# Performance work log

Hardware: AMD Instinct MI355X
Metric: run time of the kernel (lower is better)

## Reference

```python
import jax, jax.numpy as jnp
import numpy as np

N_NODES = 50000


def gcn_conv(x, W, b, row, col, n):
    """PyG GCNConv with default add_self_loops=True, normalize=True.
    out[i] = sum_{e: col[e]=i} d^-1/2[row[e]] d^-1/2[i] * (x@W)[row[e]]
             + d^-1[i]*(x@W)[i] + b,  where d = in-degree + 1 (self-loop).
    """
    x_lin = x @ W                                   # [n, out_ch]
    ones = jnp.ones(row.shape[0], dtype=x.dtype)
    deg = jax.ops.segment_sum(ones, col, num_segments=n) + 1.0  # self-loop
    dinv = jax.lax.rsqrt(deg)                       # deg >= 1, safe
    norm = dinv[row] * dinv[col]                    # [E]
    msg = norm[:, None] * x_lin[row]                # [E, out_ch]
    agg = jax.ops.segment_sum(msg, col, num_segments=n)
    self_term = (dinv * dinv)[:, None] * x_lin      # self-loop contribution
    return agg + self_term + b


def setup_inputs() -> dict:
    key = jax.random.key(0)
    ks = jax.random.split(key, 10)
    in_ch, hid, out_ch = 128, 256, 64
    E = 800000
    x = jax.random.normal(ks[0], (N_NODES, in_ch), dtype=jnp.float32)
    edge_attr = jax.random.normal(ks[1], (E, 8), dtype=jnp.float32)  # unused by forward
    edge_index = jax.random.randint(ks[2], (2, E), 0, N_NODES, dtype=jnp.int64)
    def glorot(k, fan_in, fan_out):
        s = float(np.sqrt(6.0 / (fan_in + fan_out)))
        return jax.random.uniform(k, (fan_in, fan_out), jnp.float32, -s, s)
    return {
        "x": x,
        "edge_attr": edge_attr,
        "edge_index": edge_index,
        "W1": glorot(ks[3], in_ch, hid), "b1": jnp.zeros((hid,), jnp.float32),
        "W2": glorot(ks[4], hid, hid),  "b2": jnp.zeros((hid,), jnp.float32),
        "W3": glorot(ks[5], hid, out_ch), "b3": jnp.zeros((out_ch,), jnp.float32),
    }


def reference(x, edge_attr, edge_index, W1, b1, W2, b2, W3, b3):
    n = x.shape[0]
    row, col = edge_index[0], edge_index[1]
    h = jax.nn.sigmoid(gcn_conv(x, W1, b1, row, col, n))
    h = jax.nn.sigmoid(gcn_conv(h, W2, b2, row, col, n))
    # dropout(p=0.1) in eval mode is identity
    return gcn_conv(h, W3, b3, row, col, n)
```

## Files before the change

kernel.cpp:

```cpp
#include <hip/hip_runtime.h>
#include <hip/hip_bf16.h>

typedef __bf16 bf16x8_t __attribute__((ext_vector_type(8)));
typedef float f32x4_t __attribute__((ext_vector_type(4)));
typedef float f32x2_t __attribute__((ext_vector_type(2)));

__device__ __forceinline__ float bits2f(unsigned int u) {
    union { unsigned int u; float f; } c; c.u = u; return c.f;
}
__device__ __forceinline__ unsigned short f2bf_bits(float f) {
    __hip_bfloat16 h = __float2bfloat16(f);
    return __builtin_bit_cast(unsigned short, h);
}
__device__ __forceinline__ f32x2_t unpack_bf2(unsigned int u) {
    return (f32x2_t){bits2f(u << 16), bits2f(u & 0xffff0000u)};
}

__global__ void sentinel_fill(float* __restrict__ out, int n) {
    int i = blockIdx.x * blockDim.x + threadIdx.x;
    if (i < n) out[i] = 100.0f;
}

__global__ void detect_ei(const unsigned int* __restrict__ ei, int* __restrict__ flags) {
    int lane = threadIdx.x;
    int cz = 0;
    #pragma unroll
    for (int j = 0; j < 4; ++j) {
        int idx = lane * 4 + j;
        cz += (ei[2 * idx + 1] == 0u);
    }
    #pragma unroll
    for (int off = 32; off; off >>= 1) cz += __shfl_down(cz, off);
    if (lane == 0) flags[0] = (cz > 200);
}


__global__ void count_rank_dual(const int* __restrict__ ei, int* __restrict__ cnt,
                                int* __restrict__ rank, int E, int M,
                                const int* __restrict__ flags) {
    int e = blockIdx.x * blockDim.x + threadIdx.x;
    if (e < E) {
        int c = flags[0] ? ei[2 * E + 2 * e] : ei[E + e];
        int rk = 0;
        if ((unsigned)c < (unsigned)M) rk = atomicAdd(&cnt[c], 1);
        rank[e] = rk;
    }
}

__global__ void scan_blocks(const int* __restrict__ cnt, int* __restrict__ excl,
                            int* __restrict__ bsum, int n) {
    int tid = threadIdx.x;
    int i = blockIdx.x * 256 + tid;
    int lane = tid & 63, wv = tid >> 6;
    __shared__ int ws[4];
    int v = (i < n) ? cnt[i] : 0;
    int s = v;
    #pragma unroll
    for (int off = 1; off < 64; off <<= 1) {
        int t = __shfl_up(s, off);
        if (lane >= off) s += t;
    }
    if (lane == 63) ws[wv] = s;
    __syncthreads();
    if (tid == 0) { int a = 0; for (int q = 0; q < 4; ++q) { int t = ws[q]; ws[q] = a; a += t; } }
    __syncthreads();
    int ex = s - v + ws[wv];
    if (i < n) excl[i] = ex;
    if (tid == 255) bsum[blockIdx.x] = ex + v;
}

__global__ void scan_bsums(const int* __restrict__ bsum, int* __restrict__ boff,
                           int nb, int* __restrict__ colptr, int n) {
    int tid = threadIdx.x, lane = tid & 63, wv = tid >> 6;
    __shared__ int ws[4];
    __shared__ int carry;
    if (tid == 0) carry = 0;
    __syncthreads();
    for (int base = 0; base < nb; base += 256) {
        int i = base + tid;
        int v = (i < nb) ? bsum[i] : 0;
        int s = v;
        #pragma unroll
        for (int off = 1; off < 64; off <<= 1) {
            int t = __shfl_up(s, off);
            if (lane >= off) s += t;
        }
        if (lane == 63) ws[wv] = s;
        __syncthreads();
        if (tid == 0) { int a = carry; for (int q = 0; q < 4; ++q) { int t = ws[q]; ws[q] = a; a += t; } carry = a; }
        __syncthreads();
        int ex = s - v + ws[wv];
        if (i < nb) boff[i] = ex;
        __syncthreads();
    }
    if (tid == 0) colptr[n] = carry;
}

__global__ void scan_add_dinv(const int* __restrict__ excl, const int* __restrict__ boff,
                              const int* __restrict__ cnt, int* __restrict__ colptr,
                              float* __restrict__ dinv, int n) {
    int i = blockIdx.x * 256 + threadIdx.x;
    if (i < n) {
        colptr[i] = excl[i] + boff[blockIdx.x];
        dinv[i] = rsqrtf((float)cnt[i] + 1.0f);
    }
}

__global__ void fill_csr_part(const int* __restrict__ ei, const int* __restrict__ colptr,
                              const int* __restrict__ rank, int* __restrict__ esrc,
                              int E, int M, int psz, const int* __restrict__ flags) {
    int part = blockIdx.x & 7;
    int e = (blockIdx.x >> 3) * 256 + threadIdx.x;
    int lo = part * psz;
    int hi = lo + psz; if (hi > M) hi = M;
    if (e < E) {
        int r, c;
        if (flags[0]) { r = ei[2 * e]; c = ei[2 * E + 2 * e]; }
        else          { r = ei[e];     c = ei[E + e]; }
        if (c >= lo && c < hi && (unsigned)r < (unsigned)M) {
            int p = colptr[c] + rank[e];
            if ((unsigned)p < (unsigned)E) esrc[p] = r;
        }
    }
}

__global__ void transpose_all(const float* __restrict__ W1, const float* __restrict__ W2,
                              const float* __restrict__ W3,
                              unsigned short* __restrict__ Wt1, unsigned short* __restrict__ Wt2,
                              unsigned short* __restrict__ Wt3) {
    int i = blockIdx.x * 256 + threadIdx.x;
    if (i < 32768) {
        int k = i >> 8, n = i & 255;
        Wt1[n * 128 + k] = f2bf_bits(W1[i]);
    } else if (i < 32768 + 65536) {
        int j = i - 32768;
        int k = j >> 8, n = j & 255;
        Wt2[n * 256 + k] = f2bf_bits(W2[j]);
    } else if (i < 114688) {
        int j = i - 98304;
        int k = j >> 6, n = j & 63;
        Wt3[n * 256 + k] = f2bf_bits(W3[j]);
    }
}

__global__ void prescale_x(const float* __restrict__ x, const float* __restrict__ dinv,
                           unsigned short* __restrict__ xs, int total) {
    int i = blockIdx.x * 256 + threadIdx.x;
    if (i < total) {
        int row = i >> 7;
        xs[i] = f2bf_bits(x[i] * dinv[row]);
    }
}

template<int K, int BN, int NTOT, int EPI>
__global__ __launch_bounds__(256) void gemm_tile(
    const __bf16* __restrict__ A,
    const unsigned short* __restrict__ Bt,
    const float* __restrict__ dinv,
    const float* __restrict__ bias,
    void* __restrict__ Y,
    int M)
{
    constexpr int KS = (K > 128) ? 128 : K;
    constexpr int KP = KS + 8;
    constexpr int NT = BN / 2 / 16;
    __shared__ unsigned short Bs[BN * KP];

    const int tid  = threadIdx.x;
    const int lane = tid & 63;
    const int wave = tid >> 6;
    const int wm   = wave >> 1;
    const int wn   = wave & 1;
    const int quad = lane >> 4;
    const int l16  = lane & 15;
    const int n0   = blockIdx.y * BN;

    int mrow[4];
#pragma unroll
    for (int mt = 0; mt < 4; ++mt) {
        int r = blockIdx.x * 128 + wm * 64 + mt * 16 + l16;
        mrow[mt] = (r < M) ? r : (M - 1);
    }

    f32x4_t acc[4][NT];
#pragma unroll
    for (int mt = 0; mt < 4; ++mt)
#pragma unroll
        for (int t = 0; t < NT; ++t) acc[mt][t] = (f32x4_t){0.f, 0.f, 0.f, 0.f};

    const unsigned short* BsW = &Bs[(wn * (BN / 2)) * KP];

    for (int kh = 0; kh < K; kh += KS) {
        constexpr int CH = BN * KS / 8;
        for (int idx = tid; idx < CH; idx += 256) {
            int n  = idx / (KS / 8);
            int k8 = idx - n * (KS / 8);
            uint4 v = *(const uint4*)(Bt + (size_t)(n0 + n) * K + kh + k8 * 8);
            *(uint4*)&Bs[n * KP + k8 * 8] = v;
        }
        __syncthreads();

#pragma unroll
        for (int kc = 0; kc < KS; kc += 32) {
            bf16x8_t a[4], b[NT];
#pragma unroll
            for (int mt = 0; mt < 4; ++mt)
                a[mt] = *(const bf16x8_t*)(A + (size_t)mrow[mt] * K + kh + kc + quad * 8);
#pragma unroll
            for (int t = 0; t < NT; ++t)
                b[t] = *(const bf16x8_t*)&BsW[(t * 16 + l16) * KP + kc + quad * 8];
#pragma unroll
            for (int mt = 0; mt < 4; ++mt)
#pragma unroll
                for (int t = 0; t < NT; ++t)
                    acc[mt][t] = __builtin_amdgcn_mfma_f32_16x16x32_bf16(a[mt], b[t], acc[mt][t], 0, 0, 0);
        }
        if (kh + KS < K) __syncthreads();
    }

    float bv[NT];
    if constexpr (EPI == 1) {
#pragma unroll
        for (int t = 0; t < NT; ++t)
            bv[t] = bias[n0 + wn * (BN / 2) + t * 16 + l16];
    }

#pragma unroll
    for (int mt = 0; mt < 4; ++mt) {
        int rowbase = blockIdx.x * 128 + wm * 64 + mt * 16 + quad * 4;
#pragma unroll
        for (int r = 0; r < 4; ++r) {
            int rrow = rowbase + r;
            if (rrow < M) {
                if constexpr (EPI == 0) {
                    float dv = dinv[rrow];
#pragma unroll
                    for (int t = 0; t < NT; ++t) {
                        int ccol = n0 + wn * (BN / 2) + t * 16 + l16;
                        ((__hip_bfloat16*)Y)[(size_t)rrow * NTOT + ccol] =
                            __float2bfloat16(acc[mt][t][r] * dv);
                    }
                } else if constexpr (EPI == 1) {
#pragma unroll
                    for (int t = 0; t < NT; ++t) {
                        int ccol = n0 + wn * (BN / 2) + t * 16 + l16;
                        float o = acc[mt][t][r] + bv[t];
                        o = 1.f / (1.f + __expf(-o));
                        ((__hip_bfloat16*)Y)[(size_t)rrow * NTOT + ccol] = __float2bfloat16(o);
                    }
                } else {
                    float dv = dinv[rrow];
#pragma unroll
                    for (int t = 0; t < NT; ++t) {
                        int ccol = n0 + wn * (BN / 2) + t * 16 + l16;
                        float o = acc[mt][t][r] * dv;
                        int pk = __builtin_amdgcn_cvt_pk_fp8_f32(o, o, 0, false);
                        ((unsigned char*)Y)[(size_t)rrow * NTOT + ccol] = (unsigned char)(pk & 0xff);
                    }
                }
            }
        }
    }
}

__global__ __launch_bounds__(256) void aggregate_fp8_v2(
    const unsigned char* __restrict__ Y8,
    const int* __restrict__ colptr,
    const int* __restrict__ esrc,
    const float* __restrict__ dinv,
    const float* __restrict__ bias,
    unsigned short* __restrict__ H,
    int M, int Etot)
{
    const int lane = threadIdx.x & 63;
    const int wave = threadIdx.x >> 6;
    int node = blockIdx.x * 4 + wave;
    if (node >= M) return;

    int s = colptr[node];
    int e = colptr[node + 1];
    if (s < 0) s = 0;
    if (e > Etot) e = Etot;
    if (e < s) e = s;

    const char* Yb = (const char*)Y8;
    const unsigned lb = (unsigned)(lane * 4);

    f32x2_t a0 = {0.f, 0.f}, a1 = {0.f, 0.f};

    {
        unsigned u = *(const unsigned*)(Yb + (((unsigned)node) << 8) + lb);
        a0 += __builtin_amdgcn_cvt_pk_f32_fp8(u, false);
        a1 += __builtin_amdgcn_cvt_pk_f32_fp8(u, true);
    }
#pragma unroll 4
    for (int t = s; t < e; ++t) {
        unsigned off = (((unsigned)esrc[t]) << 8) + lb;
        unsigned u = *(const unsigned*)(Yb + off);
        a0 += __builtin_amdgcn_cvt_pk_f32_fp8(u, false);
        a1 += __builtin_amdgcn_cvt_pk_f32_fp8(u, true);
    }

    float dv = dinv[node];
    float4 bv = *(const float4*)(bias + lane * 4);
    float o0 = a0[0] * dv + bv.x;
    float o1 = a0[1] * dv + bv.y;
    float o2 = a1[0] * dv + bv.z;
    float o3 = a1[1] * dv + bv.w;
    o0 = 1.f / (1.f + __expf(-o0));
    o1 = 1.f / (1.f + __expf(-o1));
    o2 = 1.f / (1.f + __expf(-o2));
    o3 = 1.f / (1.f + __expf(-o3));
    uint2 st;
    st.x = (unsigned)f2bf_bits(o0) | ((unsigned)f2bf_bits(o1) << 16);
    st.y = (unsigned)f2bf_bits(o2) | ((unsigned)f2bf_bits(o3) << 16);
    *(uint2*)(H + (size_t)node * 256 + lane * 4) = st;
}

__global__ __launch_bounds__(256) void aggregate_bf16_128_v2(
    const unsigned short* __restrict__ Yin,
    const int* __restrict__ colptr,
    const int* __restrict__ esrc,
    const float* __restrict__ dinv,
    unsigned short* __restrict__ Hout,
    int M, int Etot)
{
    const int lane = threadIdx.x & 63;
    const int wave = threadIdx.x >> 6;
    int node = blockIdx.x * 4 + wave;
    if (node >= M) return;

    int s = colptr[node];
    int e = colptr[node + 1];
    if (s < 0) s = 0;
    if (e > Etot) e = Etot;
    if (e < s) e = s;

    const char* Yb = (const char*)Yin;
    const unsigned lb = (unsigned)(lane * 4);

    f32x2_t a = {0.f, 0.f};
    {
        unsigned u = *(const unsigned*)(Yb + (((unsigned)node) << 8) + lb);
        a += unpack_bf2(u);
    }
#pragma unroll 4
    for (int t = s; t < e; ++t) {
        unsigned off = (((unsigned)esrc[t]) << 8) + lb;
        unsigned u = *(const unsigned*)(Yb + off);
        a += unpack_bf2(u);
    }

    float dv = dinv[node];
    unsigned st = (unsigned)f2bf_bits(a[0] * dv) | ((unsigned)f2bf_bits(a[1] * dv) << 16);
    *(unsigned*)((char*)Hout + (size_t)node * 256 + lane * 4) = st;
}

__global__ __launch_bounds__(256) void aggregate_bf16_64_f32(
    const unsigned short* __restrict__ Yin,
    const int* __restrict__ colptr,
    const int* __restrict__ esrc,
    const float* __restrict__ dinv,
    const float* __restrict__ bias,
    float* __restrict__ out,
    int M, int Etot)
{
    const int lane = threadIdx.x & 63;
    const int wave = threadIdx.x >> 6;
    const int l5 = lane & 31;
    const int g  = lane >> 5;
    int node = blockIdx.x * 4 + wave;
    if (node >= M) return;

    int s = colptr[node];
    int e = colptr[node + 1];
    if (s < 0) s = 0;
    if (e > Etot) e = Etot;
    if (e < s) e = s;

    const char* Yb = (const char*)Yin;
    const unsigned lb = (unsigned)(l5 * 4);

    f32x2_t a = {0.f, 0.f};
    if (g == 0) {
        unsigned u = *(const unsigned*)(Yb + (((unsigned)node) << 7) + lb);
        a += unpack_bf2(u);
    }
#pragma unroll 4
    for (int t = s + g; t < e; t += 2) {
        unsigned off = (((unsigned)esrc[t]) << 7) + lb;
        unsigned u = *(const unsigned*)(Yb + off);
        a += unpack_bf2(u);
    }

    a[0] += __shfl_xor(a[0], 32);
    a[1] += __shfl_xor(a[1], 32);

    if (g == 0) {
        float dv = dinv[node];
        float2 bv = *(const float2*)(bias + l5 * 2);
        float2 st;
        st.x = a[0] * dv + bv.x;
        st.y = a[1] * dv + bv.y;
        *(float2*)(out + (size_t)node * 64 + l5 * 2) = st;
    }
}


extern "C" void kernel_launch(void* const* d_in, const int* in_sizes, int n_in,
                              void* d_out, int out_size, void* d_ws, size_t ws_size,
                              hipStream_t stream)
{
    int iEI = 2, iW1 = 3, iB1 = 4, iW2 = 5, iB2 = 6, iW3 = 7, iB3 = 8;
    if (n_in == 8) { iEI = 1; iW1 = 2; iB1 = 3; iW2 = 4; iB2 = 5; iW3 = 6; iB3 = 7; }

    const float* x  = (const float*)d_in[0];
    const int* ei   = (const int*)d_in[iEI];
    const float* W1 = (const float*)d_in[iW1];
    const float* b1 = (const float*)d_in[iB1];
    const float* W2 = (const float*)d_in[iW2];
    const float* b2 = (const float*)d_in[iB2];
    const float* W3 = (const float*)d_in[iW3];
    const float* b3 = (const float*)d_in[iB3];

    const int M = in_sizes[0] / 128;
    const int E = in_sizes[iEI] / 2;
    const int NB = (M + 255) / 256;
    const int PSZ = (M + 7) / 8;

    auto rnd = [](size_t b) { return (b + 255) & ~(size_t)255; };
    size_t needed = rnd(64 * 4)
                  + rnd((size_t)M * 4) * 2
                  + rnd((size_t)(M + 1) * 4)
                  + rnd((size_t)M * 4)
                  + rnd((size_t)(NB + 1) * 4) * 2
                  + rnd((size_t)E * 4) * 2
                  + rnd((size_t)256 * 128 * 2)
                  + rnd((size_t)256 * 256 * 2)
                  + rnd((size_t)64 * 256 * 2)
                  + rnd((size_t)M * 256 * 2) * 2;
    if (ws_size < needed) {
        sentinel_fill<<<(out_size + 255) / 256, 256, 0, stream>>>((float*)d_out, out_size);
        return;
    }

    char* p = (char*)d_ws;
    auto alloc = [&](size_t bytes) {
        char* r = p;
        p += (bytes + 255) & ~(size_t)255;
        return r;
    };
    int* flags  = (int*)alloc(64 * 4);
    float* dinv = (float*)alloc((size_t)M * 4);
    int* cnt    = (int*)alloc((size_t)M * 4);
    int* colptr = (int*)alloc((size_t)(M + 1) * 4);
    int* excl   = (int*)alloc((size_t)M * 4);
    int* bsum   = (int*)alloc((size_t)(NB + 1) * 4);
    int* boff   = (int*)alloc((size_t)(NB + 1) * 4);
    int* esrc   = (int*)alloc((size_t)E * 4);
    int* rank   = (int*)alloc((size_t)E * 4);
    unsigned short* Wt1 = (unsigned short*)alloc((size_t)256 * 128 * 2);
    unsigned short* Wt2 = (unsigned short*)alloc((size_t)256 * 256 * 2);
    unsigned short* Wt3 = (unsigned short*)alloc((size_t)64 * 256 * 2);
    __hip_bfloat16* ybuf = (__hip_bfloat16*)alloc((size_t)M * 256 * 2);
    __hip_bfloat16* hbuf = (__hip_bfloat16*)alloc((size_t)M * 256 * 2);

    unsigned short* xs = (unsigned short*)ybuf;
    unsigned short* xa = (unsigned short*)ybuf + (size_t)M * 128;
    unsigned char*  y8 = (unsigned char*)ybuf;

    detect_ei<<<1, 64, 0, stream>>>((const unsigned int*)ei, flags);

    hipMemsetAsync(cnt, 0, (size_t)M * 4, stream);
    count_rank_dual<<<(E + 255) / 256, 256, 0, stream>>>(ei, cnt, rank, E, M, flags);
    scan_blocks<<<NB, 256, 0, stream>>>(cnt, excl, bsum, M);
    scan_bsums<<<1, 256, 0, stream>>>(bsum, boff, NB, colptr, M);
    scan_add_dinv<<<NB, 256, 0, stream>>>(excl, boff, cnt, colptr, dinv, M);
    fill_csr_part<<<((E + 255) / 256) * 8, 256, 0, stream>>>(
        ei, colptr, rank, esrc, E, M, PSZ, flags);
    transpose_all<<<(114688 + 255) / 256, 256, 0, stream>>>(W1, W2, W3, Wt1, Wt2, Wt3);

    int gmb = (M + 127) / 128;
    int ga  = (M + 3) / 4;

    prescale_x<<<((M * 128) + 255) / 256, 256, 0, stream>>>(x, dinv, xs, M * 128);
    aggregate_bf16_128_v2<<<ga, 256, 0, stream>>>(
        xs, colptr, esrc, dinv, xa, M, E);
    gemm_tile<128, 128, 256, 1><<<dim3(gmb, 2), 256, 0, stream>>>(
        (const __bf16*)xa, Wt1, dinv, b1, hbuf, M);
    gemm_tile<256, 128, 256, 2><<<dim3(gmb, 2), 256, 0, stream>>>(
        (const __bf16*)hbuf, Wt2, dinv, b2, y8, M);
    aggregate_fp8_v2<<<ga, 256, 0, stream>>>(
        y8, colptr, esrc, dinv, b2, (unsigned short*)hbuf, M, E);
    gemm_tile<256, 64, 64, 0><<<dim3(gmb, 1), 256, 0, stream>>>(
        (const __bf16*)hbuf, Wt3, dinv, b3, ybuf, M);
    aggregate_bf16_64_f32<<<ga, 256, 0, stream>>>(
        (const unsigned short*)ybuf, colptr, esrc, dinv, b3, (float*)d_out, M, E);
}
```

Before: 343.9 us.

## Split gather features into 128-byte column chunks and parallelize edges within waves

```diff
diff --git a/kernel.cpp b/kernel.cpp
--- a/kernel.cpp
+++ b/kernel.cpp
@@ -14,6 +14,12 @@
 }
 __device__ __forceinline__ f32x2_t unpack_bf2(unsigned int u) {
     return (f32x2_t){bits2f(u << 16), bits2f(u & 0xffff0000u)};
+}
+__device__ __forceinline__ f32x2_t xsw(f32x2_t v, int off) {
+    f32x2_t r;
+    r[0] = __shfl_xor(v[0], off);
+    r[1] = __shfl_xor(v[1], off);
+    return r;
 }
 
 __global__ void sentinel_fill(float* __restrict__ out, int n) {
@@ -35,12 +41,17 @@
 }
 
 
-__global__ void count_rank_dual(const int* __restrict__ ei, int* __restrict__ cnt,
-                                int* __restrict__ rank, int E, int M,
-                                const int* __restrict__ flags) {
+__global__ void count_rank_dual2(const int* __restrict__ ei, int* __restrict__ cnt,
+                                 int* __restrict__ rank, int* __restrict__ c32,
+                                 int* __restrict__ r32, int E, int M,
+                                 const int* __restrict__ flags) {
     int e = blockIdx.x * blockDim.x + threadIdx.x;
     if (e < E) {
-        int c = flags[0] ? ei[2 * E + 2 * e] : ei[E + e];
+        int r, c;
+        if (flags[0]) { r = ei[2 * e]; c = ei[2 * E + 2 * e]; }
+        else          { r = ei[e];     c = ei[E + e]; }
+        c32[e] = c;
+        r32[e] = r;
         int rk = 0;
         if ((unsigned)c < (unsigned)M) rk = atomicAdd(&cnt[c], 1);
         rank[e] = rk;
@@ -106,20 +117,21 @@
     }
 }
 
-__global__ void fill_csr_part(const int* __restrict__ ei, const int* __restrict__ colptr,
-                              const int* __restrict__ rank, int* __restrict__ esrc,
-                              int E, int M, int psz, const int* __restrict__ flags) {
+__global__ void fill_csr_part2(const int* __restrict__ c32, const int* __restrict__ r32,
+                               const int* __restrict__ colptr, const int* __restrict__ rank,
+                               int* __restrict__ esrc, int E, int M, int psz) {
     int part = blockIdx.x & 7;
     int e = (blockIdx.x >> 3) * 256 + threadIdx.x;
     int lo = part * psz;
     int hi = lo + psz; if (hi > M) hi = M;
     if (e < E) {
-        int r, c;
-        if (flags[0]) { r = ei[2 * e]; c = ei[2 * E + 2 * e]; }
-        else          { r = ei[e];     c = ei[E + e]; }
-        if (c >= lo && c < hi && (unsigned)r < (unsigned)M) {
-            int p = colptr[c] + rank[e];
-            if ((unsigned)p < (unsigned)E) esrc[p] = r;
+        int c = c32[e];
+        if (c >= lo && c < hi) {
+            int r = r32[e];
+            if ((unsigned)r < (unsigned)M) {
+                int p = colptr[c] + rank[e];
+                if ((unsigned)p < (unsigned)E) esrc[p] = r;
+            }
         }
     }
 }
@@ -144,11 +156,13 @@
 }
 
 __global__ void prescale_x(const float* __restrict__ x, const float* __restrict__ dinv,
-                           unsigned short* __restrict__ xs, int total) {
+                           unsigned short* __restrict__ xs, int M, int total) {
     int i = blockIdx.x * 256 + threadIdx.x;
     if (i < total) {
         int row = i >> 7;
-        xs[i] = f2bf_bits(x[i] * dinv[row]);
+        int k = i & 127;
+        xs[(size_t)(k >> 6) * ((size_t)M * 64) + (size_t)row * 64 + (k & 63)] =
+            f2bf_bits(x[i] * dinv[row]);
     }
 }
 
@@ -255,7 +269,9 @@
                         int ccol = n0 + wn * (BN / 2) + t * 16 + l16;
                         float o = acc[mt][t][r] * dv;
                         int pk = __builtin_amdgcn_cvt_pk_fp8_f32(o, o, 0, false);
-                        ((unsigned char*)Y)[(size_t)rrow * NTOT + ccol] = (unsigned char)(pk & 0xff);
+                        size_t choff = (size_t)(ccol >> 7) * ((size_t)M * 128)
+                                     + (size_t)rrow * 128 + (ccol & 127);
+                        ((unsigned char*)Y)[choff] = (unsigned char)(pk & 0xff);
                     }
                 }
             }
@@ -263,18 +279,23 @@
     }
 }
 
-__global__ __launch_bounds__(256) void aggregate_fp8_v2(
-    const unsigned char* __restrict__ Y8,
+__global__ __launch_bounds__(256) void aggregate_fp8_c2(
+    const unsigned char* __restrict__ Y8c,
     const int* __restrict__ colptr,
     const int* __restrict__ esrc,
     const float* __restrict__ dinv,
     const float* __restrict__ bias,
     unsigned short* __restrict__ H,
-    int M, int Etot)
+    int M, int Etot, int nbx)
 {
     const int lane = threadIdx.x & 63;
     const int wave = threadIdx.x >> 6;
-    int node = blockIdx.x * 4 + wave;
+    const int sub = lane & 15;
+    const int grp = lane >> 4;
+    int bx = blockIdx.x;
+    int chunk = (bx >= nbx) ? 1 : 0;
+    if (chunk) bx -= nbx;
+    int node = bx * 4 + wave;
     if (node >= M) return;
 
     int s = colptr[node];
@@ -282,52 +303,70 @@
     if (s < 0) s = 0;
     if (e > Etot) e = Etot;
     if (e < s) e = s;
-
-    const char* Yb = (const char*)Y8;
-    const unsigned lb = (unsigned)(lane * 4);
-
-    f32x2_t a0 = {0.f, 0.f}, a1 = {0.f, 0.f};
-
-    {
-        unsigned u = *(const unsigned*)(Yb + (((unsigned)node) << 8) + lb);
-        a0 += __builtin_amdgcn_cvt_pk_f32_fp8(u, false);
-        a1 += __builtin_amdgcn_cvt_pk_f32_fp8(u, true);
-    }
-#pragma unroll 4
-    for (int t = s; t < e; ++t) {
-        unsigned off = (((unsigned)esrc[t]) << 8) + lb;
-        unsigned u = *(const unsigned*)(Yb + off);
-        a0 += __builtin_amdgcn_cvt_pk_f32_fp8(u, false);
-        a1 += __builtin_amdgcn_cvt_pk_f32_fp8(u, true);
-    }
-
-    float dv = dinv[node];
-    float4 bv = *(const float4*)(bias + lane * 4);
-    float o0 = a0[0] * dv + bv.x;
-    float o1 = a0[1] * dv + bv.y;
-    float o2 = a1[0] * dv + bv.z;
-    float o3 = a1[1] * dv + bv.w;
-    o0 = 1.f / (1.f + __expf(-o0));
-    o1 = 1.f / (1.f + __expf(-o1));
-    o2 = 1.f / (1.f + __expf(-o2));
-    o3 = 1.f / (1.f + __expf(-o3));
-    uint2 st;
-    st.x = (unsigned)f2bf_bits(o0) | ((unsigned)f2bf_bits(o1) << 16);
-    st.y = (unsigned)f2bf_bits(o2) | ((unsigned)f2bf_bits(o3) << 16);
-    *(uint2*)(H + (size_t)node * 256 + lane * 4) = st;
-}
-
-__global__ __launch_bounds__(256) void aggregate_bf16_128_v2(
-    const unsigned short* __restrict__ Yin,
+    int n = e - s;
+
+    const char* Yb = (const char*)(Y8c + (size_t)chunk * ((size_t)M * 128));
+    const unsigned lb = (unsigned)(sub * 8);
+
+    f32x2_t a0 = {0.f, 0.f}, a1 = {0.f, 0.f}, a2 = {0.f, 0.f}, a3 = {0.f, 0.f};
+
+    if (grp == 0) {
+        uint2 u = *(const uint2*)(Yb + ((unsigned)node) * 128u + lb);
+        a0 += __builtin_amdgcn_cvt_pk_f32_fp8(u.x, false);
+        a1 += __builtin_amdgcn_cvt_pk_f32_fp8(u.x, true);
+        a2 += __builtin_amdgcn_cvt_pk_f32_fp8(u.y, false);
+        a3 += __builtin_amdgcn_cvt_pk_f32_fp8(u.y, true);
+    }
+#pragma unroll 2
+    for (int t = grp; t < n; t += 4) {
+        unsigned off = ((unsigned)esrc[s + t]) * 128u + lb;
+        uint2 u = *(const uint2*)(Yb + off);
+        a0 += __builtin_amdgcn_cvt_pk_f32_fp8(u.x, false);
+        a1 += __builtin_amdgcn_cvt_pk_f32_fp8(u.x, true);
+        a2 += __builtin_amdgcn_cvt_pk_f32_fp8(u.y, false);
+        a3 += __builtin_amdgcn_cvt_pk_f32_fp8(u.y, true);
+    }
+
+    a0 += xsw(a0, 16); a1 += xsw(a1, 16); a2 += xsw(a2, 16); a3 += xsw(a3, 16);
+    a0 += xsw(a0, 32); a1 += xsw(a1, 32); a2 += xsw(a2, 32); a3 += xsw(a3, 32);
+
+    if (grp == 0) {
+        float dv = dinv[node];
+        int chb = chunk * 128 + sub * 8;
+        float4 b0 = *(const float4*)(bias + chb);
+        float4 b1 = *(const float4*)(bias + chb + 4);
+        float o[8];
+        o[0] = a0[0] * dv + b0.x; o[1] = a0[1] * dv + b0.y;
+        o[2] = a1[0] * dv + b0.z; o[3] = a1[1] * dv + b0.w;
+        o[4] = a2[0] * dv + b1.x; o[5] = a2[1] * dv + b1.y;
+        o[6] = a3[0] * dv + b1.z; o[7] = a3[1] * dv + b1.w;
+        #pragma unroll
+        for (int k = 0; k < 8; ++k) o[k] = 1.f / (1.f + __expf(-o[k]));
+        uint4 st;
+        st.x = (unsigned)f2bf_bits(o[0]) | ((unsigned)f2bf_bits(o[1]) << 16);
+        st.y = (unsigned)f2bf_bits(o[2]) | ((unsigned)f2bf_bits(o[3]) << 16);
+        st.z = (unsigned)f2bf_bits(o[4]) | ((unsigned)f2bf_bits(o[5]) << 16);
+        st.w = (unsigned)f2bf_bits(o[6]) | ((unsigned)f2bf_bits(o[7]) << 16);
+        *(uint4*)(H + (size_t)node * 256 + chb) = st;
+    }
+}
+
+__global__ __launch_bounds__(256) void aggregate_bf16_c2(
+    const unsigned short* __restrict__ Xc,
     const int* __restrict__ colptr,
     const int* __restrict__ esrc,
     const float* __restrict__ dinv,
     unsigned short* __restrict__ Hout,
-    int M, int Etot)
+    int M, int Etot, int nbx)
 {
     const int lane = threadIdx.x & 63;
     const int wave = threadIdx.x >> 6;
-    int node = blockIdx.x * 4 + wave;
+    const int sub = lane & 15;
+    const int grp = lane >> 4;
+    int bx = blockIdx.x;
+    int chunk = (bx >= nbx) ? 1 : 0;
+    if (chunk) bx -= nbx;
+    int node = bx * 4 + wave;
     if (node >= M) return;
 
     int s = colptr[node];
@@ -335,28 +374,39 @@
     if (s < 0) s = 0;
     if (e > Etot) e = Etot;
     if (e < s) e = s;
-
-    const char* Yb = (const char*)Yin;
-    const unsigned lb = (unsigned)(lane * 4);
-
-    f32x2_t a = {0.f, 0.f};
-    {
-        unsigned u = *(const unsigned*)(Yb + (((unsigned)node) << 8) + lb);
-        a += unpack_bf2(u);
-    }
-#pragma unroll 4
-    for (int t = s; t < e; ++t) {
-        unsigned off = (((unsigned)esrc[t]) << 8) + lb;
-        unsigned u = *(const unsigned*)(Yb + off);
-        a += unpack_bf2(u);
-    }
-
-    float dv = dinv[node];
-    unsigned st = (unsigned)f2bf_bits(a[0] * dv) | ((unsigned)f2bf_bits(a[1] * dv) << 16);
-    *(unsigned*)((char*)Hout + (size_t)node * 256 + lane * 4) = st;
-}
-
-__global__ __launch_bounds__(256) void aggregate_bf16_64_f32(
+    int n = e - s;
+
+    const char* Yb = (const char*)(Xc + (size_t)chunk * ((size_t)M * 64));
+    const unsigned lb = (unsigned)(sub * 8);
+
+    f32x2_t a0 = {0.f, 0.f}, a1 = {0.f, 0.f};
+
+    if (grp == 0) {
+        uint2 u = *(const uint2*)(Yb + ((unsigned)node) * 128u + lb);
+        a0 += unpack_bf2(u.x);
+        a1 += unpack_bf2(u.y);
+    }
+#pragma unroll 2
+    for (int t = grp; t < n; t += 4) {
+        unsigned off = ((unsigned)esrc[s + t]) * 128u + lb;
+        uint2 u = *(const uint2*)(Yb + off);
+        a0 += unpack_bf2(u.x);
+        a1 += unpack_bf2(u.y);
+    }
+
+    a0 += xsw(a0, 16); a1 += xsw(a1, 16);
+    a0 += xsw(a0, 32); a1 += xsw(a1, 32);
+
+    if (grp == 0) {
+        float dv = dinv[node];
+        uint2 st;
+        st.x = (unsigned)f2bf_bits(a0[0] * dv) | ((unsigned)f2bf_bits(a0[1] * dv) << 16);
+        st.y = (unsigned)f2bf_bits(a1[0] * dv) | ((unsigned)f2bf_bits(a1[1] * dv) << 16);
+        *(uint2*)(Hout + (size_t)node * 128 + chunk * 64 + sub * 4) = st;
+    }
+}
+
+__global__ __launch_bounds__(256) void aggregate_bf16_64_v3(
     const unsigned short* __restrict__ Yin,
     const int* __restrict__ colptr,
     const int* __restrict__ esrc,
@@ -367,8 +417,8 @@
 {
     const int lane = threadIdx.x & 63;
     const int wave = threadIdx.x >> 6;
-    const int l5 = lane & 31;
-    const int g  = lane >> 5;
+    const int sub = lane & 15;
+    const int grp = lane >> 4;
     int node = blockIdx.x * 4 + wave;
     if (node >= M) return;
 
@@ -377,32 +427,38 @@
     if (s < 0) s = 0;
     if (e > Etot) e = Etot;
     if (e < s) e = s;
+    int n = e - s;
 
     const char* Yb = (const char*)Yin;
-    const unsigned lb = (unsigned)(l5 * 4);
-
-    f32x2_t a = {0.f, 0.f};
-    if (g == 0) {
-        unsigned u = *(const unsigned*)(Yb + (((unsigned)node) << 7) + lb);
-        a += unpack_bf2(u);
-    }
-#pragma unroll 4
-    for (int t = s + g; t < e; t += 2) {
-        unsigned off = (((unsigned)esrc[t]) << 7) + lb;
-        unsigned u = *(const unsigned*)(Yb + off);
-        a += unpack_bf2(u);
-    }
-
-    a[0] += __shfl_xor(a[0], 32);
-    a[1] += __shfl_xor(a[1], 32);
-
-    if (g == 0) {
+    const unsigned lb = (unsigned)(sub * 8);
+
+    f32x2_t a0 = {0.f, 0.f}, a1 = {0.f, 0.f};
+
+    if (grp == 0) {
+        uint2 u = *(const uint2*)(Yb + ((unsigned)node) * 128u + lb);
+        a0 += unpack_bf2(u.x);
+        a1 += unpack_bf2(u.y);
+    }
+#pragma unroll 2
+    for (int t = grp; t < n; t += 4) {
+        unsigned off = ((unsigned)esrc[s + t]) * 128u + lb;
+        uint2 u = *(const uint2*)(Yb + off);
+        a0 += unpack_bf2(u.x);
+        a1 += unpack_bf2(u.y);
+    }
+
+    a0 += xsw(a0, 16); a1 += xsw(a1, 16);
+    a0 += xsw(a0, 32); a1 += xsw(a1, 32);
+
+    if (grp == 0) {
         float dv = dinv[node];
-        float2 bv = *(const float2*)(bias + l5 * 2);
-        float2 st;
-        st.x = a[0] * dv + bv.x;
-        st.y = a[1] * dv + bv.y;
-        *(float2*)(out + (size_t)node * 64 + l5 * 2) = st;
+        float4 bv = *(const float4*)(bias + sub * 4);
+        float4 st;
+        st.x = a0[0] * dv + bv.x;
+        st.y = a0[1] * dv + bv.y;
+        st.z = a1[0] * dv + bv.z;
+        st.w = a1[1] * dv + bv.w;
+        *(float4*)(out + (size_t)node * 64 + sub * 4) = st;
     }
 }
 
@@ -434,7 +490,7 @@
                   + rnd((size_t)(M + 1) * 4)
                   + rnd((size_t)M * 4)
                   + rnd((size_t)(NB + 1) * 4) * 2
-                  + rnd((size_t)E * 4) * 2
+                  + rnd((size_t)E * 4) * 4
                   + rnd((size_t)256 * 128 * 2)
                   + rnd((size_t)256 * 256 * 2)
                   + rnd((size_t)64 * 256 * 2)
@@ -459,6 +515,8 @@
     int* boff   = (int*)alloc((size_t)(NB + 1) * 4);
     int* esrc   = (int*)alloc((size_t)E * 4);
     int* rank   = (int*)alloc((size_t)E * 4);
+    int* c32    = (int*)alloc((size_t)E * 4);
+    int* r32    = (int*)alloc((size_t)E * 4);
     unsigned short* Wt1 = (unsigned short*)alloc((size_t)256 * 128 * 2);
     unsigned short* Wt2 = (unsigned short*)alloc((size_t)256 * 256 * 2);
     unsigned short* Wt3 = (unsigned short*)alloc((size_t)64 * 256 * 2);
@@ -472,28 +530,28 @@
     detect_ei<<<1, 64, 0, stream>>>((const unsigned int*)ei, flags);
 
     hipMemsetAsync(cnt, 0, (size_t)M * 4, stream);
-    count_rank_dual<<<(E + 255) / 256, 256, 0, stream>>>(ei, cnt, rank, E, M, flags);
+    count_rank_dual2<<<(E + 255) / 256, 256, 0, stream>>>(ei, cnt, rank, c32, r32, E, M, flags);
     scan_blocks<<<NB, 256, 0, stream>>>(cnt, excl, bsum, M);
     scan_bsums<<<1, 256, 0, stream>>>(bsum, boff, NB, colptr, M);
     scan_add_dinv<<<NB, 256, 0, stream>>>(excl, boff, cnt, colptr, dinv, M);
-    fill_csr_part<<<((E + 255) / 256) * 8, 256, 0, stream>>>(
-        ei, colptr, rank, esrc, E, M, PSZ, flags);
+    fill_csr_part2<<<((E + 255) / 256) * 8, 256, 0, stream>>>(
+        c32, r32, colptr, rank, esrc, E, M, PSZ);
     transpose_all<<<(114688 + 255) / 256, 256, 0, stream>>>(W1, W2, W3, Wt1, Wt2, Wt3);
 
     int gmb = (M + 127) / 128;
     int ga  = (M + 3) / 4;
 
-    prescale_x<<<((M * 128) + 255) / 256, 256, 0, stream>>>(x, dinv, xs, M * 128);
-    aggregate_bf16_128_v2<<<ga, 256, 0, stream>>>(
-        xs, colptr, esrc, dinv, xa, M, E);
+    prescale_x<<<((M * 128) + 255) / 256, 256, 0, stream>>>(x, dinv, xs, M, M * 128);
+    aggregate_bf16_c2<<<2 * ga, 256, 0, stream>>>(
+        xs, colptr, esrc, dinv, xa, M, E, ga);
     gemm_tile<128, 128, 256, 1><<<dim3(gmb, 2), 256, 0, stream>>>(
         (const __bf16*)xa, Wt1, dinv, b1, hbuf, M);
     gemm_tile<256, 128, 256, 2><<<dim3(gmb, 2), 256, 0, stream>>>(
         (const __bf16*)hbuf, Wt2, dinv, b2, y8, M);
-    aggregate_fp8_v2<<<ga, 256, 0, stream>>>(
-        y8, colptr, esrc, dinv, b2, (unsigned short*)hbuf, M, E);
+    aggregate_fp8_c2<<<2 * ga, 256, 0, stream>>>(
+        y8, colptr, esrc, dinv, b2, (unsigned short*)hbuf, M, E, ga);
     gemm_tile<256, 64, 64, 0><<<dim3(gmb, 1), 256, 0, stream>>>(
         (const __bf16*)hbuf, Wt3, dinv, b3, ybuf, M);
-    aggregate_bf16_64_f32<<<ga, 256, 0, stream>>>(
+    aggregate_bf16_64_v3<<<ga, 256, 0, stream>>>(
         (const unsigned short*)ybuf, colptr, esrc, dinv, b3, (float*)d_out, M, E);
 }
```

Result: slower. 369.8 us (+7.5%).

## Software-pipeline neighbor gathers in aggregation kernels and cache int32 edge indices

Applied to the files above, without the earlier changes.

```diff
diff --git a/kernel.cpp b/kernel.cpp
--- a/kernel.cpp
+++ b/kernel.cpp
@@ -35,12 +35,17 @@
 }
 
 
-__global__ void count_rank_dual(const int* __restrict__ ei, int* __restrict__ cnt,
-                                int* __restrict__ rank, int E, int M,
-                                const int* __restrict__ flags) {
+__global__ void count_rank_dual2(const int* __restrict__ ei, int* __restrict__ cnt,
+                                 int* __restrict__ rank, int* __restrict__ c32,
+                                 int* __restrict__ r32, int E, int M,
+                                 const int* __restrict__ flags) {
     int e = blockIdx.x * blockDim.x + threadIdx.x;
     if (e < E) {
-        int c = flags[0] ? ei[2 * E + 2 * e] : ei[E + e];
+        int r, c;
+        if (flags[0]) { r = ei[2 * e]; c = ei[2 * E + 2 * e]; }
+        else          { r = ei[e];     c = ei[E + e]; }
+        c32[e] = c;
+        r32[e] = r;
         int rk = 0;
         if ((unsigned)c < (unsigned)M) rk = atomicAdd(&cnt[c], 1);
         rank[e] = rk;
@@ -106,20 +111,21 @@
     }
 }
 
-__global__ void fill_csr_part(const int* __restrict__ ei, const int* __restrict__ colptr,
-                              const int* __restrict__ rank, int* __restrict__ esrc,
-                              int E, int M, int psz, const int* __restrict__ flags) {
+__global__ void fill_csr_part2(const int* __restrict__ c32, const int* __restrict__ r32,
+                               const int* __restrict__ colptr, const int* __restrict__ rank,
+                               int* __restrict__ esrc, int E, int M, int psz) {
     int part = blockIdx.x & 7;
     int e = (blockIdx.x >> 3) * 256 + threadIdx.x;
     int lo = part * psz;
     int hi = lo + psz; if (hi > M) hi = M;
     if (e < E) {
-        int r, c;
-        if (flags[0]) { r = ei[2 * e]; c = ei[2 * E + 2 * e]; }
-        else          { r = ei[e];     c = ei[E + e]; }
-        if (c >= lo && c < hi && (unsigned)r < (unsigned)M) {
-            int p = colptr[c] + rank[e];
-            if ((unsigned)p < (unsigned)E) esrc[p] = r;
+        int c = c32[e];
+        if (c >= lo && c < hi) {
+            int r = r32[e];
+            if ((unsigned)r < (unsigned)M) {
+                int p = colptr[c] + rank[e];
+                if ((unsigned)p < (unsigned)E) esrc[p] = r;
+            }
         }
     }
 }
@@ -263,7 +269,7 @@
     }
 }
 
-__global__ __launch_bounds__(256) void aggregate_fp8_v2(
+__global__ __launch_bounds__(256) void aggregate_fp8_v4(
     const unsigned char* __restrict__ Y8,
     const int* __restrict__ colptr,
     const int* __restrict__ esrc,
@@ -282,24 +288,58 @@
     if (s < 0) s = 0;
     if (e > Etot) e = Etot;
     if (e < s) e = s;
+    int n = e - s;
 
     const char* Yb = (const char*)Y8;
     const unsigned lb = (unsigned)(lane * 4);
 
+    unsigned su = *(const unsigned*)(Yb + (((unsigned)node) << 8) + lb);
+
     f32x2_t a0 = {0.f, 0.f}, a1 = {0.f, 0.f};
 
-    {
-        unsigned u = *(const unsigned*)(Yb + (((unsigned)node) << 8) + lb);
-        a0 += __builtin_amdgcn_cvt_pk_f32_fp8(u, false);
-        a1 += __builtin_amdgcn_cvt_pk_f32_fp8(u, true);
-    }
-#pragma unroll 4
-    for (int t = s; t < e; ++t) {
-        unsigned off = (((unsigned)esrc[t]) << 8) + lb;
+    auto gather8 = [&](unsigned* u, int base) {
+        #pragma unroll
+        for (int k = 0; k < 8; ++k) {
+            unsigned off = (((unsigned)esrc[s + base + k]) << 8) + lb;
+            u[k] = *(const unsigned*)(Yb + off);
+        }
+    };
+    auto acc8 = [&](const unsigned* u) {
+        #pragma unroll
+        for (int k = 0; k < 8; ++k) {
+            a0 += __builtin_amdgcn_cvt_pk_f32_fp8(u[k], false);
+            a1 += __builtin_amdgcn_cvt_pk_f32_fp8(u[k], true);
+        }
+    };
+
+    unsigned ua[8], ub[8];
+    int NB = n >> 3;
+    if (NB > 0) {
+        gather8(ua, 0);
+        int i = 1;
+        for (; i + 1 < NB; i += 2) {
+            gather8(ub, i << 3);
+            acc8(ua);
+            gather8(ua, (i + 1) << 3);
+            acc8(ub);
+        }
+        if (i < NB) {
+            gather8(ub, i << 3);
+            acc8(ua);
+            acc8(ub);
+        } else {
+            acc8(ua);
+        }
+    }
+    #pragma unroll 2
+    for (int t = NB << 3; t < n; ++t) {
+        unsigned off = (((unsigned)esrc[s + t]) << 8) + lb;
         unsigned u = *(const unsigned*)(Yb + off);
         a0 += __builtin_amdgcn_cvt_pk_f32_fp8(u, false);
         a1 += __builtin_amdgcn_cvt_pk_f32_fp8(u, true);
     }
+    a0 += __builtin_amdgcn_cvt_pk_f32_fp8(su, false);
+    a1 += __builtin_amdgcn_cvt_pk_f32_fp8(su, true);
 
     float dv = dinv[node];
     float4 bv = *(const float4*)(bias + lane * 4);
@@ -317,7 +357,7 @@
     *(uint2*)(H + (size_t)node * 256 + lane * 4) = st;
 }
 
-__global__ __launch_bounds__(256) void aggregate_bf16_128_v2(
+__global__ __launch_bounds__(256) void aggregate_bf16_128_v4(
     const unsigned short* __restrict__ Yin,
     const int* __restrict__ colptr,
     const int* __restrict__ esrc,
@@ -335,28 +375,60 @@
     if (s < 0) s = 0;
     if (e > Etot) e = Etot;
     if (e < s) e = s;
+    int n = e - s;
 
     const char* Yb = (const char*)Yin;
     const unsigned lb = (unsigned)(lane * 4);
 
+    unsigned su = *(const unsigned*)(Yb + (((unsigned)node) << 8) + lb);
+
     f32x2_t a = {0.f, 0.f};
-    {
-        unsigned u = *(const unsigned*)(Yb + (((unsigned)node) << 8) + lb);
-        a += unpack_bf2(u);
-    }
-#pragma unroll 4
-    for (int t = s; t < e; ++t) {
-        unsigned off = (((unsigned)esrc[t]) << 8) + lb;
+
+    auto gather8 = [&](unsigned* u, int base) {
+        #pragma unroll
+        for (int k = 0; k < 8; ++k) {
+            unsigned off = (((unsigned)esrc[s + base + k]) << 8) + lb;
+            u[k] = *(const unsigned*)(Yb + off);
+        }
+    };
+    auto acc8 = [&](const unsigned* u) {
+        #pragma unroll
+        for (int k = 0; k < 8; ++k) a += unpack_bf2(u[k]);
+    };
+
+    unsigned ua[8], ub[8];
+    int NB = n >> 3;
+    if (NB > 0) {
+        gather8(ua, 0);
+        int i = 1;
+        for (; i + 1 < NB; i += 2) {
+            gather8(ub, i << 3);
+            acc8(ua);
+            gather8(ua, (i + 1) << 3);
+            acc8(ub);
+        }
+        if (i < NB) {
+            gather8(ub, i << 3);
+            acc8(ua);
+            acc8(ub);
+        } else {
+            acc8(ua);
+        }
+    }
+    #pragma unroll 2
+    for (int t = NB << 3; t < n; ++t) {
+        unsigned off = (((unsigned)esrc[s + t]) << 8) + lb;
         unsigned u = *(const unsigned*)(Yb + off);
         a += unpack_bf2(u);
     }
+    a += unpack_bf2(su);
 
     float dv = dinv[node];
     unsigned st = (unsigned)f2bf_bits(a[0] * dv) | ((unsigned)f2bf_bits(a[1] * dv) << 16);
     *(unsigned*)((char*)Hout + (size_t)node * 256 + lane * 4) = st;
 }
 
-__global__ __launch_bounds__(256) void aggregate_bf16_64_f32(
+__global__ __launch_bounds__(256) void aggregate_bf16_64_v4(
     const unsigned short* __restrict__ Yin,
     const int* __restrict__ colptr,
     const int* __restrict__ esrc,
@@ -377,21 +449,53 @@
     if (s < 0) s = 0;
     if (e > Etot) e = Etot;
     if (e < s) e = s;
+    int n = e - s;
 
     const char* Yb = (const char*)Yin;
     const unsigned lb = (unsigned)(l5 * 4);
 
+    unsigned su = 0;
+    if (g == 0) su = *(const unsigned*)(Yb + (((unsigned)node) << 7) + lb);
+
     f32x2_t a = {0.f, 0.f};
-    if (g == 0) {
-        unsigned u = *(const unsigned*)(Yb + (((unsigned)node) << 7) + lb);
-        a += unpack_bf2(u);
-    }
-#pragma unroll 4
-    for (int t = s + g; t < e; t += 2) {
-        unsigned off = (((unsigned)esrc[t]) << 7) + lb;
+
+    auto gather4 = [&](unsigned* u, int base) {
+        #pragma unroll
+        for (int k = 0; k < 4; ++k) {
+            unsigned off = (((unsigned)esrc[s + base + 2 * k + g]) << 7) + lb;
+            u[k] = *(const unsigned*)(Yb + off);
+        }
+    };
+    auto acc4 = [&](const unsigned* u) {
+        #pragma unroll
+        for (int k = 0; k < 4; ++k) a += unpack_bf2(u[k]);
+    };
+
+    unsigned ua[4], ub[4];
+    int NB = n >> 3;
+    if (NB > 0) {
+        gather4(ua, 0);
+        int i = 1;
+        for (; i + 1 < NB; i += 2) {
+            gather4(ub, i << 3);
+            acc4(ua);
+            gather4(ua, (i + 1) << 3);
+            acc4(ub);
+        }
+        if (i < NB) {
+            gather4(ub, i << 3);
+            acc4(ua);
+            acc4(ub);
+        } else {
+            acc4(ua);
+        }
+    }
+    for (int t = NB << 3; t + g < n; t += 2) {
+        unsigned off = (((unsigned)esrc[s + t + g]) << 7) + lb;
         unsigned u = *(const unsigned*)(Yb + off);
         a += unpack_bf2(u);
     }
+    if (g == 0) a += unpack_bf2(su);
 
     a[0] += __shfl_xor(a[0], 32);
     a[1] += __shfl_xor(a[1], 32);
@@ -434,7 +538,7 @@
                   + rnd((size_t)(M + 1) * 4)
                   + rnd((size_t)M * 4)
                   + rnd((size_t)(NB + 1) * 4) * 2
-                  + rnd((size_t)E * 4) * 2
+                  + rnd((size_t)E * 4) * 4
                   + rnd((size_t)256 * 128 * 2)
                   + rnd((size_t)256 * 256 * 2)
                   + rnd((size_t)64 * 256 * 2)
@@ -459,6 +563,8 @@
     int* boff   = (int*)alloc((size_t)(NB + 1) * 4);
     int* esrc   = (int*)alloc((size_t)E * 4);
     int* rank   = (int*)alloc((size_t)E * 4);
+    int* c32    = (int*)alloc((size_t)E * 4);
+    int* r32    = (int*)alloc((size_t)E * 4);
     unsigned short* Wt1 = (unsigned short*)alloc((size_t)256 * 128 * 2);
     unsigned short* Wt2 = (unsigned short*)alloc((size_t)256 * 256 * 2);
     unsigned short* Wt3 = (unsigned short*)alloc((size_t)64 * 256 * 2);
@@ -472,28 +578,28 @@
     detect_ei<<<1, 64, 0, stream>>>((const unsigned int*)ei, flags);
 
     hipMemsetAsync(cnt, 0, (size_t)M * 4, stream);
-    count_rank_dual<<<(E + 255) / 256, 256, 0, stream>>>(ei, cnt, rank, E, M, flags);
+    count_rank_dual2<<<(E + 255) / 256, 256, 0, stream>>>(ei, cnt, rank, c32, r32, E, M, flags);
     scan_blocks<<<NB, 256, 0, stream>>>(cnt, excl, bsum, M);
     scan_bsums<<<1, 256, 0, stream>>>(bsum, boff, NB, colptr, M);
     scan_add_dinv<<<NB, 256, 0, stream>>>(excl, boff, cnt, colptr, dinv, M);
-    fill_csr_part<<<((E + 255) / 256) * 8, 256, 0, stream>>>(
-        ei, colptr, rank, esrc, E, M, PSZ, flags);
+    fill_csr_part2<<<((E + 255) / 256) * 8, 256, 0, stream>>>(
+        c32, r32, colptr, rank, esrc, E, M, PSZ);
     transpose_all<<<(114688 + 255) / 256, 256, 0, stream>>>(W1, W2, W3, Wt1, Wt2, Wt3);
 
     int gmb = (M + 127) / 128;
     int ga  = (M + 3) / 4;
 
     prescale_x<<<((M * 128) + 255) / 256, 256, 0, stream>>>(x, dinv, xs, M * 128);
-    aggregate_bf16_128_v2<<<ga, 256, 0, stream>>>(
+    aggregate_bf16_128_v4<<<ga, 256, 0, stream>>>(
         xs, colptr, esrc, dinv, xa, M, E);
     gemm_tile<128, 128, 256, 1><<<dim3(gmb, 2), 256, 0, stream>>>(
         (const __bf16*)xa, Wt1, dinv, b1, hbuf, M);
     gemm_tile<256, 128, 256, 2><<<dim3(gmb, 2), 256, 0, stream>>>(
         (const __bf16*)hbuf, Wt2, dinv, b2, y8, M);
-    aggregate_fp8_v2<<<ga, 256, 0, stream>>>(
+    aggregate_fp8_v4<<<ga, 256, 0, stream>>>(
         y8, colptr, esrc, dinv, b2, (unsigned short*)hbuf, M, E);
     gemm_tile<256, 64, 64, 0><<<dim3(gmb, 1), 256, 0, stream>>>(
         (const __bf16*)hbuf, Wt3, dinv, b3, ybuf, M);
-    aggregate_bf16_64_f32<<<ga, 256, 0, stream>>>(
+    aggregate_bf16_64_v4<<<ga, 256, 0, stream>>>(
         (const unsigned short*)ybuf, colptr, esrc, dinv, b3, (float*)d_out, M, E);
 }
```

New measurement: 343.4 us. Within noise of the previous version (-0.1%).
